# Optimization experiments

Hardware: AMD Instinct MI355X
Metric: run time of the kernel (lower is better)

## Reference

```python
import jax, jax.numpy as jnp
import numpy as np

B, S, D_IN, D_OUT = 4, 2048, 1024, 1024


def setup_inputs() -> dict:
    key = jax.random.key(0)
    kx, kq, kk, kv = jax.random.split(key, 4)
    scale = 1.0 / np.sqrt(D_IN)
    return {
        "x": jax.random.normal(kx, (B, S, D_IN), dtype=jnp.float32),
        "W_q": jax.random.normal(kq, (D_IN, D_OUT), dtype=jnp.float32) * scale,
        "W_k": jax.random.normal(kk, (D_IN, D_OUT), dtype=jnp.float32) * scale,
        "W_v": jax.random.normal(kv, (D_IN, D_OUT), dtype=jnp.float32) * scale,
    }


def reference(x, W_q, W_k, W_v):
    # QKV projections (Linear without bias): [B,S,D_out]
    q = jnp.einsum("bsd,de->bse", x, W_q)
    k = jnp.einsum("bsd,de->bse", x, W_k)
    v = jnp.einsum("bsd,de->bse", x, W_v)

    # Raw scores [B,S,S], causal mask (strict upper triangle -> -inf),
    # then scale by sqrt(d_k) and softmax, matching the torch order of ops.
    scores = jnp.einsum("bqd,bkd->bqk", q, k)
    seq = scores.shape[-1]
    causal = jnp.triu(jnp.ones((seq, seq), dtype=bool), k=1)
    scores = jnp.where(causal[None, :, :], -jnp.inf, scores)
    attn = jax.nn.softmax(scores / jnp.sqrt(jnp.asarray(q.shape[-1], scores.dtype)), axis=-1)
    # dropout p=0.0 -> identity (eval semantics)
    return jnp.einsum("bqk,bkd->bqd", attn, v)
```

## Files before the change

### kernel.cpp

```cpp
#include <hip/hip_runtime.h>

typedef unsigned short u16;
typedef __bf16 bf16x8 __attribute__((ext_vector_type(8)));
typedef float f32x4 __attribute__((ext_vector_type(4)));

__device__ __forceinline__ u16 f2bf(float f) {
    union { float f; unsigned int u; } v; v.f = f;
    unsigned int u = v.u;
    return (u16)((u + 0x7FFFu + ((u >> 16) & 1u)) >> 16);
}

__device__ __forceinline__ void load_lds16(const void* g, void* l) {
    __builtin_amdgcn_global_load_lds(
        (const __attribute__((address_space(1))) unsigned int*)g,
        (__attribute__((address_space(3))) unsigned int*)l,
        16, 0, 0);
}

__global__ void __launch_bounds__(256) prep_kernel(
    const float4* __restrict__ X, u16* __restrict__ xb,
    const float* __restrict__ Wq, const float* __restrict__ Wk,
    const float* __restrict__ Wv,
    u16* __restrict__ Oq, u16* __restrict__ Ok, u16* __restrict__ Ov,
    float* __restrict__ rowsum) {
    __shared__ float tile[32][33];
    const int bid = blockIdx.x, tid = threadIdx.x;
    if (bid < 8192) {
        int idx = bid * 256 + tid;
        float4 v = X[idx];
        ushort4 o;
        o.x = f2bf(v.x); o.y = f2bf(v.y); o.z = f2bf(v.z); o.w = f2bf(v.w);
        *(ushort4*)(xb + (size_t)idx * 4) = o;
    } else if (bid < 11264) {
        int id = bid - 8192;
        int zz = id >> 10;
        const float* W = (zz == 0) ? Wq : (zz == 1) ? Wk : Wv;
        u16* O = (zz == 0) ? Oq : (zz == 1) ? Ok : Ov;
        int n0 = (id & 31) * 32, k0 = ((id >> 5) & 31) * 32;
        int tx = tid & 31, ty = tid >> 5;
        #pragma unroll
        for (int j = 0; j < 32; j += 8)
            tile[ty + j][tx] = W[(size_t)(k0 + ty + j) * 1024 + n0 + tx];
        __syncthreads();
        #pragma unroll
        for (int j = 0; j < 32; j += 8)
            O[(size_t)(n0 + ty + j) * 1024 + k0 + tx] = f2bf(tile[tx][ty + j]);
    } else {
        rowsum[(bid - 11264) * 256 + tid] = 0.f;
    }
}

template <int MODE>
__global__ void __launch_bounds__(512) gemm_nt(
    const u16* __restrict__ xb, const u16* __restrict__ WqT,
    const u16* __restrict__ WkT, const u16* __restrict__ WvT,
    u16* __restrict__ Q, u16* __restrict__ Kb,
    u16* __restrict__ Vt, u16* __restrict__ S,
    float* __restrict__ rowsum, float* __restrict__ out) {

    int mtile, ntile, z;
    const u16 *A, *B;

    if (MODE == 0) {
        int L = blockIdx.x;
        int c = L & 7, t = (L >> 3) & 7, hi = L >> 6;
        int p = hi * 8 + c;
        z = p >> 6; mtile = p & 63; ntile = t;
        A = xb;
        B = (z == 0) ? WqT : (z == 1) ? WkT : WvT;
    } else if (MODE == 1) {
        int id2 = blockIdx.x;
        z = id2 / 192;
        int r = id2 - z * 192;
        int c = r & 7, g = r >> 3;
        if (g <= c)            { mtile = c;     ntile = g; }
        else if (g < 2*c + 10) { mtile = c + 8; ntile = g - (c + 1); }
        else return;
        A = Q  + (size_t)z * (2048 * 1024);
        B = Kb + (size_t)z * (2048 * 1024);
    } else {
        int L = blockIdx.x;
        ntile = L & 7;
        int j = L >> 3;
        z = j & 3; mtile = 15 - (j >> 2);
        A = S  + (size_t)z * (2048 * 2048);
        B = Vt + (size_t)z * (1024 * 2048);
    }

    const int LDA = (MODE == 2) ? 2048 : 1024;
    const int kiters = (MODE == 2) ? (mtile + 1) * 2 : 16;

    __shared__ __align__(16) u16 As[128 * 64];
    __shared__ __align__(16) u16 Bs[128 * 64];

    const int tid = threadIdx.x;
    const int lane = tid & 63;
    const int wave = tid >> 6;
    const int wr = wave >> 2, wc = wave & 3;

    const int r0 = tid >> 2;
    const int kb = (((tid & 3) ^ ((r0 >> 1) & 3))) * 16;

    const char* gA = (const char*)(A + (size_t)(mtile * 128 + r0) * LDA) + kb;
    const char* gB = (const char*)(B + (size_t)(ntile * 128 + r0) * LDA) + kb;

    char* lA = (char*)As + tid * 16;
    char* lB = (char*)Bs + tid * 16;

    f32x4 acc[4][2] = {};

    const int quad = lane >> 4;
    const int l16 = lane & 15;
    const int ch = quad ^ ((l16 >> 1) & 3);
    const int aoff = (wr * 64 + l16) * 32 + ch * 8;
    const int boff = (wc * 32 + l16) * 32 + ch * 8;

    for (int kt = 0; kt < kiters; ++kt) {
        load_lds16(gA,      lA);
        load_lds16(gA + 64, lA + 8192);
        load_lds16(gB,      lB);
        load_lds16(gB + 64, lB + 8192);
        gA += 128; gB += 128;
        __syncthreads();

        #pragma unroll
        for (int h = 0; h < 2; ++h) {
            const u16* ap = As + h * 4096 + aoff;
            const u16* bp = Bs + h * 4096 + boff;
            bf16x8 af[4], bfv[2];
            #pragma unroll
            for (int r = 0; r < 4; ++r) af[r] = *(const bf16x8*)(ap + r * 512);
            #pragma unroll
            for (int c = 0; c < 2; ++c) bfv[c] = *(const bf16x8*)(bp + c * 512);
            #pragma unroll
            for (int r = 0; r < 4; ++r)
                #pragma unroll
                for (int c = 0; c < 2; ++c)
                    acc[r][c] = __builtin_amdgcn_mfma_f32_16x16x32_bf16(
                        af[r], bfv[c], acc[r][c], 0, 0, 0);
        }
        __syncthreads();
    }

    const int grow0 = mtile * 128 + wr * 64 + quad * 4;
    const int gcol0 = ntile * 128 + wc * 32 + l16;

    if (MODE == 0) {
        if (z < 2) {
            u16* C = z ? Kb : Q;
            #pragma unroll
            for (int r = 0; r < 4; ++r)
                #pragma unroll
                for (int c = 0; c < 2; ++c)
                    #pragma unroll
                    for (int i = 0; i < 4; ++i)
                        C[(size_t)(grow0 + r * 16 + i) * 1024 + gcol0 + c * 16] =
                            f2bf(acc[r][c][i]);
        } else {
            #pragma unroll
            for (int r = 0; r < 4; ++r) {
                int m0 = grow0 + r * 16;
                int b = m0 >> 11, s0 = m0 & 2047;
                #pragma unroll
                for (int c = 0; c < 2; ++c) {
                    int d = gcol0 + c * 16;
                    ushort4 o;
                    o.x = f2bf(acc[r][c][0]); o.y = f2bf(acc[r][c][1]);
                    o.z = f2bf(acc[r][c][2]); o.w = f2bf(acc[r][c][3]);
                    *(ushort4*)(Vt + (size_t)b * (1024 * 2048) + (size_t)d * 2048 + s0) = o;
                }
            }
        }
    } else if (MODE == 1) {
        u16* C = S + (size_t)z * (2048 * 2048);
        float* rs = rowsum + z * 2048;
        const bool diag = (ntile == mtile);
        float rsum[4][4];
        #pragma unroll
        for (int r = 0; r < 4; ++r)
            #pragma unroll
            for (int i = 0; i < 4; ++i) rsum[r][i] = 0.f;
        #pragma unroll
        for (int r = 0; r < 4; ++r)
            #pragma unroll
            for (int c = 0; c < 2; ++c)
                #pragma unroll
                for (int i = 0; i < 4; ++i) {
                    int grow = grow0 + r * 16 + i;
                    int gcol = gcol0 + c * 16;
                    float e = 0.f;
                    if (!diag || gcol <= grow)
                        e = __expf(acc[r][c][i] * 0.03125f - 12.0f);
                    C[(size_t)grow * 2048 + gcol] = f2bf(e);
                    rsum[r][i] += e;
                }
        #pragma unroll
        for (int r = 0; r < 4; ++r)
            #pragma unroll
            for (int i = 0; i < 4; ++i) {
                float s = rsum[r][i];
                s += __shfl_xor(s, 1, 64);
                s += __shfl_xor(s, 2, 64);
                s += __shfl_xor(s, 4, 64);
                s += __shfl_xor(s, 8, 64);
                if (l16 == 0)
                    atomicAdd(&rs[grow0 + r * 16 + i], s);
            }
    } else {
        const float* rs = rowsum + z * 2048;
        float* C = out + (size_t)z * (2048 * 1024);
        #pragma unroll
        for (int r = 0; r < 4; ++r)
            #pragma unroll
            for (int i = 0; i < 4; ++i) {
                int grow = grow0 + r * 16 + i;
                float inv = 1.0f / rs[grow];
                #pragma unroll
                for (int c = 0; c < 2; ++c)
                    C[(size_t)grow * 1024 + gcol0 + c * 16] = acc[r][c][i] * inv;
            }
    }
}

extern "C" void kernel_launch(void* const* d_in, const int* in_sizes, int n_in,
                              void* d_out, int out_size, void* d_ws, size_t ws_size,
                              hipStream_t stream) {
    const float* x  = (const float*)d_in[0];
    const float* Wq = (const float*)d_in[1];
    const float* Wk = (const float*)d_in[2];
    const float* Wv = (const float*)d_in[3];
    float* out = (float*)d_out;
    char* ws = (char*)d_ws;
    const size_t Mi = 1u << 20;

    u16* xb  = (u16*)(ws);
    u16* WqT = (u16*)(ws + 16 * Mi);
    u16* WkT = (u16*)(ws + 18 * Mi);
    u16* WvT = (u16*)(ws + 20 * Mi);
    u16* Q   = (u16*)(ws + 22 * Mi);
    u16* Kb  = (u16*)(ws + 38 * Mi);
    u16* Vt  = (u16*)(ws + 54 * Mi);
    u16* S   = (u16*)(ws + 70 * Mi);
    float* rowsum = (float*)(ws + 102 * Mi);

    prep_kernel<<<11296, 256, 0, stream>>>(
        (const float4*)x, xb, Wq, Wk, Wv, WqT, WkT, WvT, rowsum);

    gemm_nt<0><<<1536, 512, 0, stream>>>(xb, WqT, WkT, WvT, Q, Kb, Vt, S, rowsum, out);

    gemm_nt<1><<<768, 512, 0, stream>>>(xb, WqT, WkT, WvT, Q, Kb, Vt, S, rowsum, out);

    gemm_nt<2><<<512, 512, 0, stream>>>(xb, WqT, WkT, WvT, Q, Kb, Vt, S, rowsum, out);
}
```

Measured before the change: 219.4 us.

## Split-K long PV row tiles and halve QK^T tile width for load balance

The P·V GEMM now splits the eight longest row-tiles (mtile 8..15) into two K halves, each accumulated into the output with float atomics, using a constant schedule table that orders work classes longest-first. The prep kernel zero-fills the output rows those split tiles cover. The QK^T score GEMM uses 128x64 tiles instead of 128x128, doubling its grid to improve occupancy and tail balance, and the rowsum accumulation switches to unsafeAtomicAdd. This targets load imbalance across the causal triangle, at the cost of extra atomic traffic, output zeroing, and repeated A-tile loads in the score GEMM.

```diff
diff --git a/kernel.cpp b/kernel.cpp
--- a/kernel.cpp
+++ b/kernel.cpp
@@ -17,12 +17,15 @@
         16, 0, 0);
 }
 
+__constant__ unsigned char cls_m[24] = {15,15,7,14,14,13,13,6,12,12,11,11,5,10,10,9,9,4,8,8,3,2,1,0};
+__constant__ unsigned char cls_h[24] = { 0, 1,2, 0, 1, 0, 1,2, 0, 1, 0, 1,2, 0, 1,0,1,2,0,1,2,2,2,2};
+
 __global__ void __launch_bounds__(256) prep_kernel(
     const float4* __restrict__ X, u16* __restrict__ xb,
     const float* __restrict__ Wq, const float* __restrict__ Wk,
     const float* __restrict__ Wv,
     u16* __restrict__ Oq, u16* __restrict__ Ok, u16* __restrict__ Ov,
-    float* __restrict__ rowsum) {
+    float* __restrict__ rowsum, float4* __restrict__ outz) {
     __shared__ float tile[32][33];
     const int bid = blockIdx.x, tid = threadIdx.x;
     if (bid < 8192) {
@@ -45,8 +48,13 @@
         #pragma unroll
         for (int j = 0; j < 32; j += 8)
             O[(size_t)(n0 + ty + j) * 1024 + k0 + tx] = f2bf(tile[tx][ty + j]);
+    } else if (bid < 11296) {
+        rowsum[(bid - 11264) * 256 + tid] = 0.f;
     } else {
-        rowsum[(bid - 11264) * 256 + tid] = 0.f;
+        int i = bid - 11296;
+        int z = i >> 10;
+        outz[(size_t)z * (2048 * 1024 / 4) + (1024 * 1024 / 4)
+             + (size_t)(i & 1023) * 256 + tid] = make_float4(0.f, 0.f, 0.f, 0.f);
     }
 }
 
@@ -58,7 +66,8 @@
     u16* __restrict__ Vt, u16* __restrict__ S,
     float* __restrict__ rowsum, float* __restrict__ out) {
 
-    int mtile, ntile, z;
+    int mtile, ntile, z, nh = 0, kbeg = 0, kcnt;
+    bool split = false;
     const u16 *A, *B;
 
     if (MODE == 0) {
@@ -68,30 +77,42 @@
         z = p >> 6; mtile = p & 63; ntile = t;
         A = xb;
         B = (z == 0) ? WqT : (z == 1) ? WkT : WvT;
+        kcnt = 16;
     } else if (MODE == 1) {
         int id2 = blockIdx.x;
-        z = id2 / 192;
-        int r = id2 - z * 192;
+        nh = (id2 >= 768) ? 1 : 0;
+        int rr = id2 - nh * 768;
+        z = rr / 192;
+        int r = rr - z * 192;
         int c = r & 7, g = r >> 3;
         if (g <= c)            { mtile = c;     ntile = g; }
         else if (g < 2*c + 10) { mtile = c + 8; ntile = g - (c + 1); }
         else return;
         A = Q  + (size_t)z * (2048 * 1024);
         B = Kb + (size_t)z * (2048 * 1024);
+        kcnt = 16;
     } else {
         int L = blockIdx.x;
         ntile = L & 7;
         int j = L >> 3;
-        z = j & 3; mtile = 15 - (j >> 2);
+        z = j & 3;
+        int ci = j >> 2;
+        mtile = cls_m[ci];
+        int h = cls_h[ci];
+        split = (h != 2);
+        kbeg = split ? h * (mtile + 1) : 0;
+        kcnt = split ? (mtile + 1) : (mtile + 1) * 2;
         A = S  + (size_t)z * (2048 * 2048);
         B = Vt + (size_t)z * (1024 * 2048);
     }
 
     const int LDA = (MODE == 2) ? 2048 : 1024;
-    const int kiters = (MODE == 2) ? (mtile + 1) * 2 : 16;
+    constexpr int NC    = (MODE == 1) ? 1 : 2;
+    constexpr int BROWS = (MODE == 1) ? 64 : 128;
+    constexpr int BHALF = BROWS * 32;
 
     __shared__ __align__(16) u16 As[128 * 64];
-    __shared__ __align__(16) u16 Bs[128 * 64];
+    __shared__ __align__(16) u16 Bs[BROWS * 64];
 
     const int tid = threadIdx.x;
     const int lane = tid & 63;
@@ -101,41 +122,43 @@
     const int r0 = tid >> 2;
     const int kb = (((tid & 3) ^ ((r0 >> 1) & 3))) * 16;
 
-    const char* gA = (const char*)(A + (size_t)(mtile * 128 + r0) * LDA) + kb;
-    const char* gB = (const char*)(B + (size_t)(ntile * 128 + r0) * LDA) + kb;
+    const char* gA = (const char*)(A + (size_t)(mtile * 128 + r0) * LDA) + kb + kbeg * 128;
+    const char* gB = (const char*)(B + (size_t)(ntile * 128 + nh * 64 + r0) * LDA) + kb + kbeg * 128;
 
     char* lA = (char*)As + tid * 16;
     char* lB = (char*)Bs + tid * 16;
 
-    f32x4 acc[4][2] = {};
+    f32x4 acc[4][NC] = {};
 
     const int quad = lane >> 4;
     const int l16 = lane & 15;
     const int ch = quad ^ ((l16 >> 1) & 3);
     const int aoff = (wr * 64 + l16) * 32 + ch * 8;
-    const int boff = (wc * 32 + l16) * 32 + ch * 8;
-
-    for (int kt = 0; kt < kiters; ++kt) {
+    const int boff = (wc * 16 * NC + l16) * 32 + ch * 8;
+
+    for (int kt = 0; kt < kcnt; ++kt) {
         load_lds16(gA,      lA);
         load_lds16(gA + 64, lA + 8192);
-        load_lds16(gB,      lB);
-        load_lds16(gB + 64, lB + 8192);
+        if (MODE != 1 || tid < 256) {
+            load_lds16(gB,      lB);
+            load_lds16(gB + 64, lB + BHALF * 2);
+        }
         gA += 128; gB += 128;
         __syncthreads();
 
         #pragma unroll
-        for (int h = 0; h < 2; ++h) {
-            const u16* ap = As + h * 4096 + aoff;
-            const u16* bp = Bs + h * 4096 + boff;
-            bf16x8 af[4], bfv[2];
+        for (int h2 = 0; h2 < 2; ++h2) {
+            const u16* ap = As + h2 * 4096 + aoff;
+            const u16* bp = Bs + h2 * BHALF + boff;
+            bf16x8 af[4], bfv[NC];
             #pragma unroll
             for (int r = 0; r < 4; ++r) af[r] = *(const bf16x8*)(ap + r * 512);
             #pragma unroll
-            for (int c = 0; c < 2; ++c) bfv[c] = *(const bf16x8*)(bp + c * 512);
+            for (int c = 0; c < NC; ++c) bfv[c] = *(const bf16x8*)(bp + c * 512);
             #pragma unroll
             for (int r = 0; r < 4; ++r)
                 #pragma unroll
-                for (int c = 0; c < 2; ++c)
+                for (int c = 0; c < NC; ++c)
                     acc[r][c] = __builtin_amdgcn_mfma_f32_16x16x32_bf16(
                         af[r], bfv[c], acc[r][c], 0, 0, 0);
         }
@@ -143,7 +166,7 @@
     }
 
     const int grow0 = mtile * 128 + wr * 64 + quad * 4;
-    const int gcol0 = ntile * 128 + wc * 32 + l16;
+    const int gcol0 = ntile * 128 + nh * 64 + wc * 16 * NC + l16;
 
     if (MODE == 0) {
         if (z < 2) {
@@ -183,17 +206,15 @@
         #pragma unroll
         for (int r = 0; r < 4; ++r)
             #pragma unroll
-            for (int c = 0; c < 2; ++c)
-                #pragma unroll
-                for (int i = 0; i < 4; ++i) {
-                    int grow = grow0 + r * 16 + i;
-                    int gcol = gcol0 + c * 16;
-                    float e = 0.f;
-                    if (!diag || gcol <= grow)
-                        e = __expf(acc[r][c][i] * 0.03125f - 12.0f);
-                    C[(size_t)grow * 2048 + gcol] = f2bf(e);
-                    rsum[r][i] += e;
-                }
+            for (int i = 0; i < 4; ++i) {
+                int grow = grow0 + r * 16 + i;
+                int gcol = gcol0;
+                float e = 0.f;
+                if (!diag || gcol <= grow)
+                    e = __expf(acc[r][0][i] * 0.03125f - 12.0f);
+                C[(size_t)grow * 2048 + gcol] = f2bf(e);
+                rsum[r][i] += e;
+            }
         #pragma unroll
         for (int r = 0; r < 4; ++r)
             #pragma unroll
@@ -204,7 +225,7 @@
                 s += __shfl_xor(s, 4, 64);
                 s += __shfl_xor(s, 8, 64);
                 if (l16 == 0)
-                    atomicAdd(&rs[grow0 + r * 16 + i], s);
+                    unsafeAtomicAdd(&rs[grow0 + r * 16 + i], s);
             }
     } else {
         const float* rs = rowsum + z * 2048;
@@ -216,8 +237,12 @@
                 int grow = grow0 + r * 16 + i;
                 float inv = 1.0f / rs[grow];
                 #pragma unroll
-                for (int c = 0; c < 2; ++c)
-                    C[(size_t)grow * 1024 + gcol0 + c * 16] = acc[r][c][i] * inv;
+                for (int c = 0; c < 2; ++c) {
+                    float vv = acc[r][c][i] * inv;
+                    float* p = &C[(size_t)grow * 1024 + gcol0 + c * 16];
+                    if (split) unsafeAtomicAdd(p, vv);
+                    else       *p = vv;
+                }
             }
     }
 }
@@ -243,12 +268,12 @@
     u16* S   = (u16*)(ws + 70 * Mi);
     float* rowsum = (float*)(ws + 102 * Mi);
 
-    prep_kernel<<<11296, 256, 0, stream>>>(
-        (const float4*)x, xb, Wq, Wk, Wv, WqT, WkT, WvT, rowsum);
+    prep_kernel<<<15392, 256, 0, stream>>>(
+        (const float4*)x, xb, Wq, Wk, Wv, WqT, WkT, WvT, rowsum, (float4*)out);
 
     gemm_nt<0><<<1536, 512, 0, stream>>>(xb, WqT, WkT, WvT, Q, Kb, Vt, S, rowsum, out);
 
-    gemm_nt<1><<<768, 512, 0, stream>>>(xb, WqT, WkT, WvT, Q, Kb, Vt, S, rowsum, out);
-
-    gemm_nt<2><<<512, 512, 0, stream>>>(xb, WqT, WkT, WvT, Q, Kb, Vt, S, rowsum, out);
-}
+    gemm_nt<1><<<1536, 512, 0, stream>>>(xb, WqT, WkT, WvT, Q, Kb, Vt, S, rowsum, out);
+
+    gemm_nt<2><<<768, 512, 0, stream>>>(xb, WqT, WkT, WvT, Q, Kb, Vt, S, rowsum, out);
+}
```

New measurement: 255.4 us. 1.16x slower.

## Split long causal PV tiles into K halves with a combine pass

Applied to the files above, without the earlier changes.

Row tiles 8-15 of the attention-times-V GEMM are split along K into two halves. One half is written unnormalized to out and the other to a scratch buffer that reuses xb. A new combine kernel adds the halves and applies the row-sum normalization. This balances the triangular work so the longest blocks no longer dominate, at the cost of an extra 768-block grid, an extra kernel launch, and extra fp32 traffic. The row-sum atomics also switch to unsafeAtomicAdd.

```diff
diff --git a/kernel.cpp b/kernel.cpp
--- a/kernel.cpp
+++ b/kernel.cpp
@@ -16,6 +16,9 @@
         (__attribute__((address_space(3))) unsigned int*)l,
         16, 0, 0);
 }
+
+__constant__ unsigned char cls_m[24] = {15,15,7,14,14,13,13,6,12,12,11,11,5,10,10,9,9,4,8,8,3,2,1,0};
+__constant__ unsigned char cls_h[24] = { 0, 1,2, 0, 1, 0, 1,2, 0, 1, 0, 1,2, 0, 1,0,1,2,0,1,2,2,2,2};
 
 __global__ void __launch_bounds__(256) prep_kernel(
     const float4* __restrict__ X, u16* __restrict__ xb,
@@ -50,15 +53,34 @@
     }
 }
 
+__global__ void __launch_bounds__(256) combine_kernel(
+    const float4* __restrict__ P1, const float* __restrict__ rowsum,
+    float4* __restrict__ out) {
+    int b = blockIdx.x;
+    int z = b >> 10;
+    int i = (b & 1023) * 256 + threadIdx.x;
+    int r = i >> 8;
+    float inv = 1.0f / rowsum[z * 2048 + 1024 + r];
+    size_t oi = (size_t)z * (2048 * 1024 / 4) + (1024 * 1024 / 4) + i;
+    float4 a = out[oi];
+    float4 p = P1[(size_t)z * (1024 * 1024 / 4) + i];
+    a.x = (a.x + p.x) * inv;
+    a.y = (a.y + p.y) * inv;
+    a.z = (a.z + p.z) * inv;
+    a.w = (a.w + p.w) * inv;
+    out[oi] = a;
+}
+
 template <int MODE>
 __global__ void __launch_bounds__(512) gemm_nt(
     const u16* __restrict__ xb, const u16* __restrict__ WqT,
     const u16* __restrict__ WkT, const u16* __restrict__ WvT,
     u16* __restrict__ Q, u16* __restrict__ Kb,
     u16* __restrict__ Vt, u16* __restrict__ S,
-    float* __restrict__ rowsum, float* __restrict__ out) {
-
-    int mtile, ntile, z;
+    float* __restrict__ rowsum, float* __restrict__ out,
+    float* __restrict__ P1) {
+
+    int mtile, ntile, z, kbeg = 0, kiters, kh = 2;
     const u16 *A, *B;
 
     if (MODE == 0) {
@@ -68,6 +90,7 @@
         z = p >> 6; mtile = p & 63; ntile = t;
         A = xb;
         B = (z == 0) ? WqT : (z == 1) ? WkT : WvT;
+        kiters = 16;
     } else if (MODE == 1) {
         int id2 = blockIdx.x;
         z = id2 / 192;
@@ -78,20 +101,25 @@
         else return;
         A = Q  + (size_t)z * (2048 * 1024);
         B = Kb + (size_t)z * (2048 * 1024);
+        kiters = 16;
     } else {
         int L = blockIdx.x;
         ntile = L & 7;
         int j = L >> 3;
-        z = j & 3; mtile = 15 - (j >> 2);
+        z = j & 3;
+        int ci = j >> 2;
+        mtile = cls_m[ci];
+        kh = cls_h[ci];
+        kbeg = (kh != 2) ? kh * (mtile + 1) : 0;
+        kiters = (kh != 2) ? (mtile + 1) : (mtile + 1) * 2;
         A = S  + (size_t)z * (2048 * 2048);
         B = Vt + (size_t)z * (1024 * 2048);
     }
 
     const int LDA = (MODE == 2) ? 2048 : 1024;
-    const int kiters = (MODE == 2) ? (mtile + 1) * 2 : 16;
 
     __shared__ __align__(16) u16 As[128 * 64];
-    __shared__ __align__(16) u16 Bs[128 * 64];
+    __shared__ __align__(16) u16 Bs[128 * 64 + MODE * 256];
 
     const int tid = threadIdx.x;
     const int lane = tid & 63;
@@ -101,8 +129,8 @@
     const int r0 = tid >> 2;
     const int kb = (((tid & 3) ^ ((r0 >> 1) & 3))) * 16;
 
-    const char* gA = (const char*)(A + (size_t)(mtile * 128 + r0) * LDA) + kb;
-    const char* gB = (const char*)(B + (size_t)(ntile * 128 + r0) * LDA) + kb;
+    const char* gA = (const char*)(A + (size_t)(mtile * 128 + r0) * LDA) + kb + kbeg * 128;
+    const char* gB = (const char*)(B + (size_t)(ntile * 128 + r0) * LDA) + kb + kbeg * 128;
 
     char* lA = (char*)As + tid * 16;
     char* lB = (char*)Bs + tid * 16;
@@ -204,21 +232,45 @@
                 s += __shfl_xor(s, 4, 64);
                 s += __shfl_xor(s, 8, 64);
                 if (l16 == 0)
-                    atomicAdd(&rs[grow0 + r * 16 + i], s);
+                    unsafeAtomicAdd(&rs[grow0 + r * 16 + i], s);
             }
     } else {
-        const float* rs = rowsum + z * 2048;
-        float* C = out + (size_t)z * (2048 * 1024);
-        #pragma unroll
-        for (int r = 0; r < 4; ++r)
-            #pragma unroll
-            for (int i = 0; i < 4; ++i) {
-                int grow = grow0 + r * 16 + i;
-                float inv = 1.0f / rs[grow];
-                #pragma unroll
-                for (int c = 0; c < 2; ++c)
-                    C[(size_t)grow * 1024 + gcol0 + c * 16] = acc[r][c][i] * inv;
-            }
+        if (kh == 2) {
+            const float* rs = rowsum + z * 2048;
+            float* C = out + (size_t)z * (2048 * 1024);
+            #pragma unroll
+            for (int r = 0; r < 4; ++r)
+                #pragma unroll
+                for (int i = 0; i < 4; ++i) {
+                    int grow = grow0 + r * 16 + i;
+                    float inv = 1.0f / rs[grow];
+                    #pragma unroll
+                    for (int c = 0; c < 2; ++c)
+                        C[(size_t)grow * 1024 + gcol0 + c * 16] = acc[r][c][i] * inv;
+                }
+        } else if (kh == 1) {
+            float* C = out + (size_t)z * (2048 * 1024);
+            #pragma unroll
+            for (int r = 0; r < 4; ++r)
+                #pragma unroll
+                for (int i = 0; i < 4; ++i) {
+                    int grow = grow0 + r * 16 + i;
+                    #pragma unroll
+                    for (int c = 0; c < 2; ++c)
+                        C[(size_t)grow * 1024 + gcol0 + c * 16] = acc[r][c][i];
+                }
+        } else {
+            float* Pp = P1 + (size_t)z * (1024 * 1024);
+            #pragma unroll
+            for (int r = 0; r < 4; ++r)
+                #pragma unroll
+                for (int i = 0; i < 4; ++i) {
+                    int prow = grow0 + r * 16 + i - 1024;
+                    #pragma unroll
+                    for (int c = 0; c < 2; ++c)
+                        Pp[(size_t)prow * 1024 + gcol0 + c * 16] = acc[r][c][i];
+                }
+        }
     }
 }
 
@@ -242,13 +294,17 @@
     u16* Vt  = (u16*)(ws + 54 * Mi);
     u16* S   = (u16*)(ws + 70 * Mi);
     float* rowsum = (float*)(ws + 102 * Mi);
+    float* P1 = (float*)xb;
 
     prep_kernel<<<11296, 256, 0, stream>>>(
         (const float4*)x, xb, Wq, Wk, Wv, WqT, WkT, WvT, rowsum);
 
-    gemm_nt<0><<<1536, 512, 0, stream>>>(xb, WqT, WkT, WvT, Q, Kb, Vt, S, rowsum, out);
-
-    gemm_nt<1><<<768, 512, 0, stream>>>(xb, WqT, WkT, WvT, Q, Kb, Vt, S, rowsum, out);
-
-    gemm_nt<2><<<512, 512, 0, stream>>>(xb, WqT, WkT, WvT, Q, Kb, Vt, S, rowsum, out);
-}
+    gemm_nt<0><<<1536, 512, 0, stream>>>(xb, WqT, WkT, WvT, Q, Kb, Vt, S, rowsum, out, P1);
+
+    gemm_nt<1><<<768, 512, 0, stream>>>(xb, WqT, WkT, WvT, Q, Kb, Vt, S, rowsum, out, P1);
+
+    gemm_nt<2><<<768, 512, 0, stream>>>(xb, WqT, WkT, WvT, Q, Kb, Vt, S, rowsum, out, P1);
+
+    combine_kernel<<<4096, 256, 0, stream>>>(
+        (const float4*)P1, rowsum, (float4*)out);
+}
```

After: 227.7 us. 3.8% more time.

## Double-buffer LDS pipeline with 256x128 GEMM tiles and remapped grids

Applied to the files above, without the earlier changes.

Each GEMM block now covers a 256x128 output tile instead of 128x128, with 4x4 MFMA accumulators per wave. Global-to-LDS loads are double buffered: stage kt+2 is issued while MFMAs run on the current buffer, using explicit vmcnt waits and barriers. The block-index mappings for all three modes are redone for the larger tiles and for XCD locality, and the rowsum atomic is switched to unsafeAtomicAdd. The intent is to hide global load latency and raise data reuse per block. In exchange it uses more LDS and registers and launches fewer blocks, which lowers occupancy and may leave CUs idle in the causal stages.

```diff
diff --git a/kernel.cpp b/kernel.cpp
--- a/kernel.cpp
+++ b/kernel.cpp
@@ -58,92 +58,120 @@
     u16* __restrict__ Vt, u16* __restrict__ S,
     float* __restrict__ rowsum, float* __restrict__ out) {
 
-    int mtile, ntile, z;
+    int mtile, ntile, z, kiters;
     const u16 *A, *B;
 
     if (MODE == 0) {
         int L = blockIdx.x;
-        int c = L & 7, t = (L >> 3) & 7, hi = L >> 6;
-        int p = hi * 8 + c;
-        z = p >> 6; mtile = p & 63; ntile = t;
+        int xcd = L & 7;
+        int u = L >> 3;
+        z = u >> 5;
+        int v = u & 31;
+        mtile = ((v >> 3) << 3) | xcd;
+        ntile = v & 7;
         A = xb;
         B = (z == 0) ? WqT : (z == 1) ? WkT : WvT;
+        kiters = 16;
     } else if (MODE == 1) {
-        int id2 = blockIdx.x;
-        z = id2 / 192;
-        int r = id2 - z * 192;
-        int c = r & 7, g = r >> 3;
-        if (g <= c)            { mtile = c;     ntile = g; }
-        else if (g < 2*c + 10) { mtile = c + 8; ntile = g - (c + 1); }
-        else return;
+        int L = blockIdx.x;
+        z = L >> 7;
+        int w = L & 127;
+        mtile = w >> 4;
+        ntile = w & 15;
+        if (ntile > 2 * mtile + 1) return;
         A = Q  + (size_t)z * (2048 * 1024);
         B = Kb + (size_t)z * (2048 * 1024);
+        kiters = 16;
     } else {
         int L = blockIdx.x;
         ntile = L & 7;
-        int j = L >> 3;
-        z = j & 3; mtile = 15 - (j >> 2);
+        int mt = L >> 3;
+        z = mt >> 3;
+        mtile = mt & 7;
         A = S  + (size_t)z * (2048 * 2048);
         B = Vt + (size_t)z * (1024 * 2048);
+        kiters = 4 * (mtile + 1);
     }
 
     const int LDA = (MODE == 2) ? 2048 : 1024;
-    const int kiters = (MODE == 2) ? (mtile + 1) * 2 : 16;
-
-    __shared__ __align__(16) u16 As[128 * 64];
-    __shared__ __align__(16) u16 Bs[128 * 64];
-
-    const int tid = threadIdx.x;
+
+    __shared__ __align__(16) u16 As[32768];
+    __shared__ __align__(16) u16 Bs[16384 + MODE * 128];
+
+    const int tid  = threadIdx.x;
     const int lane = tid & 63;
     const int wave = tid >> 6;
-    const int wr = wave >> 2, wc = wave & 3;
+    const int wr = wave >> 1, wc = wave & 1;
 
     const int r0 = tid >> 2;
     const int kb = (((tid & 3) ^ ((r0 >> 1) & 3))) * 16;
 
-    const char* gA = (const char*)(A + (size_t)(mtile * 128 + r0) * LDA) + kb;
-    const char* gB = (const char*)(B + (size_t)(ntile * 128 + r0) * LDA) + kb;
-
-    char* lA = (char*)As + tid * 16;
-    char* lB = (char*)Bs + tid * 16;
-
-    f32x4 acc[4][2] = {};
+    const char* gA0 = (const char*)(A + (size_t)(mtile * 256 +       r0) * LDA) + kb;
+    const char* gA1 = (const char*)(A + (size_t)(mtile * 256 + 128 + r0) * LDA) + kb;
+    const char* gB  = (const char*)(B + (size_t)(ntile * 128 +       r0) * LDA) + kb;
+
+    auto STAGE = [&](int buf, int kt) {
+        const size_t off = (size_t)kt * 128;
+        char* a = (char*)As + buf * 32768 + tid * 16;
+        char* b = (char*)Bs + buf * 16384 + tid * 16;
+        load_lds16(gA0 + off,      a);
+        load_lds16(gA0 + off + 64, a + 8192);
+        load_lds16(gA1 + off,      a + 16384);
+        load_lds16(gA1 + off + 64, a + 24576);
+        load_lds16(gB  + off,      b);
+        load_lds16(gB  + off + 64, b + 8192);
+    };
 
     const int quad = lane >> 4;
-    const int l16 = lane & 15;
-    const int ch = quad ^ ((l16 >> 1) & 3);
-    const int aoff = (wr * 64 + l16) * 32 + ch * 8;
-    const int boff = (wc * 32 + l16) * 32 + ch * 8;
-
+    const int l16  = lane & 15;
+    const int ch   = quad ^ ((l16 >> 1) & 3);
+    const int aoff = (wr >> 1) * 8192 + ((wr & 1) * 64 + l16) * 32 + ch * 8;
+    const int boff = (wc * 64 + l16) * 32 + ch * 8;
+
+    f32x4 acc[4][4] = {};
+
+    STAGE(0, 0);
+    STAGE(1, 1);
+    asm volatile("s_waitcnt vmcnt(6)" ::: "memory");
+    __builtin_amdgcn_s_barrier();
+
+    int cur = 0;
     for (int kt = 0; kt < kiters; ++kt) {
-        load_lds16(gA,      lA);
-        load_lds16(gA + 64, lA + 8192);
-        load_lds16(gB,      lB);
-        load_lds16(gB + 64, lB + 8192);
-        gA += 128; gB += 128;
-        __syncthreads();
-
+        const u16* ap = As + cur * 16384 + aoff;
+        const u16* bp = Bs + cur * 8192  + boff;
+        bf16x8 af[2][4], bv[2][4];
         #pragma unroll
         for (int h = 0; h < 2; ++h) {
-            const u16* ap = As + h * 4096 + aoff;
-            const u16* bp = Bs + h * 4096 + boff;
-            bf16x8 af[4], bfv[2];
-            #pragma unroll
-            for (int r = 0; r < 4; ++r) af[r] = *(const bf16x8*)(ap + r * 512);
-            #pragma unroll
-            for (int c = 0; c < 2; ++c) bfv[c] = *(const bf16x8*)(bp + c * 512);
+            #pragma unroll
+            for (int r = 0; r < 4; ++r) af[h][r] = *(const bf16x8*)(ap + h * 4096 + r * 512);
+            #pragma unroll
+            for (int c = 0; c < 4; ++c) bv[h][c] = *(const bf16x8*)(bp + h * 4096 + c * 512);
+        }
+        asm volatile("s_waitcnt lgkmcnt(0)" ::: "memory");
+        __builtin_amdgcn_sched_barrier(0);
+        __builtin_amdgcn_s_barrier();
+        if (kt + 2 < kiters) STAGE(cur, kt + 2);
+
+        #pragma unroll
+        for (int h = 0; h < 2; ++h)
             #pragma unroll
             for (int r = 0; r < 4; ++r)
                 #pragma unroll
-                for (int c = 0; c < 2; ++c)
+                for (int c = 0; c < 4; ++c)
                     acc[r][c] = __builtin_amdgcn_mfma_f32_16x16x32_bf16(
-                        af[r], bfv[c], acc[r][c], 0, 0, 0);
+                        af[h][r], bv[h][c], acc[r][c], 0, 0, 0);
+
+        if (kt + 2 < kiters) {
+            asm volatile("s_waitcnt vmcnt(6)" ::: "memory");
+        } else {
+            asm volatile("s_waitcnt vmcnt(0)" ::: "memory");
         }
-        __syncthreads();
-    }
-
-    const int grow0 = mtile * 128 + wr * 64 + quad * 4;
-    const int gcol0 = ntile * 128 + wc * 32 + l16;
+        __builtin_amdgcn_s_barrier();
+        cur ^= 1;
+    }
+
+    const int grow0 = mtile * 256 + wr * 64 + quad * 4;
+    const int gcol0 = ntile * 128 + wc * 64 + l16;
 
     if (MODE == 0) {
         if (z < 2) {
@@ -151,7 +179,7 @@
             #pragma unroll
             for (int r = 0; r < 4; ++r)
                 #pragma unroll
-                for (int c = 0; c < 2; ++c)
+                for (int c = 0; c < 4; ++c)
                     #pragma unroll
                     for (int i = 0; i < 4; ++i)
                         C[(size_t)(grow0 + r * 16 + i) * 1024 + gcol0 + c * 16] =
@@ -162,7 +190,7 @@
                 int m0 = grow0 + r * 16;
                 int b = m0 >> 11, s0 = m0 & 2047;
                 #pragma unroll
-                for (int c = 0; c < 2; ++c) {
+                for (int c = 0; c < 4; ++c) {
                     int d = gcol0 + c * 16;
                     ushort4 o;
                     o.x = f2bf(acc[r][c][0]); o.y = f2bf(acc[r][c][1]);
@@ -174,7 +202,7 @@
     } else if (MODE == 1) {
         u16* C = S + (size_t)z * (2048 * 2048);
         float* rs = rowsum + z * 2048;
-        const bool diag = (ntile == mtile);
+        const bool maskchk = (ntile >= 2 * mtile);
         float rsum[4][4];
         #pragma unroll
         for (int r = 0; r < 4; ++r)
@@ -183,13 +211,13 @@
         #pragma unroll
         for (int r = 0; r < 4; ++r)
             #pragma unroll
-            for (int c = 0; c < 2; ++c)
+            for (int c = 0; c < 4; ++c)
                 #pragma unroll
                 for (int i = 0; i < 4; ++i) {
                     int grow = grow0 + r * 16 + i;
                     int gcol = gcol0 + c * 16;
                     float e = 0.f;
-                    if (!diag || gcol <= grow)
+                    if (!maskchk || gcol <= grow)
                         e = __expf(acc[r][c][i] * 0.03125f - 12.0f);
                     C[(size_t)grow * 2048 + gcol] = f2bf(e);
                     rsum[r][i] += e;
@@ -204,7 +232,7 @@
                 s += __shfl_xor(s, 4, 64);
                 s += __shfl_xor(s, 8, 64);
                 if (l16 == 0)
-                    atomicAdd(&rs[grow0 + r * 16 + i], s);
+                    unsafeAtomicAdd(&rs[grow0 + r * 16 + i], s);
             }
     } else {
         const float* rs = rowsum + z * 2048;
@@ -216,7 +244,7 @@
                 int grow = grow0 + r * 16 + i;
                 float inv = 1.0f / rs[grow];
                 #pragma unroll
-                for (int c = 0; c < 2; ++c)
+                for (int c = 0; c < 4; ++c)
                     C[(size_t)grow * 1024 + gcol0 + c * 16] = acc[r][c][i] * inv;
             }
     }
@@ -246,9 +274,9 @@
     prep_kernel<<<11296, 256, 0, stream>>>(
         (const float4*)x, xb, Wq, Wk, Wv, WqT, WkT, WvT, rowsum);
 
-    gemm_nt<0><<<1536, 512, 0, stream>>>(xb, WqT, WkT, WvT, Q, Kb, Vt, S, rowsum, out);
-
-    gemm_nt<1><<<768, 512, 0, stream>>>(xb, WqT, WkT, WvT, Q, Kb, Vt, S, rowsum, out);
-
-    gemm_nt<2><<<512, 512, 0, stream>>>(xb, WqT, WkT, WvT, Q, Kb, Vt, S, rowsum, out);
-}
+    gemm_nt<0><<<768, 512, 0, stream>>>(xb, WqT, WkT, WvT, Q, Kb, Vt, S, rowsum, out);
+
+    gemm_nt<1><<<512, 512, 0, stream>>>(xb, WqT, WkT, WvT, Q, Kb, Vt, S, rowsum, out);
+
+    gemm_nt<2><<<256, 512, 0, stream>>>(xb, WqT, WkT, WvT, Q, Kb, Vt, S, rowsum, out);
+}
```

Result: slower. 232.7 us (+6.1%).
